# Performance work log

Measured on AMD Instinct MI355X. Metric: run time of the kernel, lower is better.

## Reference

```python
import jax, jax.numpy as jnp
import numpy as np

B, H, S, D = 4, 16, 2048, 128

def setup_inputs() -> dict:
    key = jax.random.key(0)
    kq, kk, kv = jax.random.split(key, 3)
    q = jax.random.normal(kq, (B, H, S, D), dtype=jnp.float32)
    k = jax.random.normal(kk, (B, H, S, D), dtype=jnp.float32)
    v = jax.random.normal(kv, (B, H, S, D), dtype=jnp.float32)
    return {"q": q, "k": k, "v": v}

def reference(q, k, v):
    # scores: [B, H, S, S] -- NOTE: original module applies no 1/sqrt(D) scale
    scores = jnp.einsum("bhqd,bhkd->bhqk", q, k)
    a = jax.nn.softmax(scores, axis=-1)  # numerically stable softmax
    return jnp.einsum("bhqk,bhkd->bhqd", a, v)
```

## Files before the change

### kernel.cpp

```cpp
#include <hip/hip_runtime.h>
#include <hip/hip_bf16.h>


#define QBLK   64
#define KVBLK  64
#define DHEAD  128
#define SEQ    2048
#define KPAD   136
#define PPAD   72
#define RESCALE_THR 8.0f

typedef _Float16 f16x8 __attribute__((ext_vector_type(8)));
typedef _Float16 f16x4 __attribute__((ext_vector_type(4)));
typedef float    f32x4 __attribute__((ext_vector_type(4)));

#define AS1P(x) ((const __attribute__((address_space(1))) void*)(size_t)(x))
#define AS3P(x) ((__attribute__((address_space(3))) void*)(unsigned long long)(unsigned)(size_t)(x))

__global__ __launch_bounds__(256)
void preconv_kernel(const float* __restrict__ K, const float* __restrict__ V,
                    _Float16* __restrict__ Kp, _Float16* __restrict__ Vp) {
    const int bt = blockIdx.x;
    const size_t src = (size_t)bt * (KVBLK * DHEAD);
    const float* Kt = K + src;
    const float* Vt = V + src;
    _Float16* Ko = Kp + src;
    _Float16* Vo = Vp + src;
    #pragma unroll
    for (int j = 0; j < 4; ++j) {
        const int c = threadIdx.x + 256 * j;
        {
            const int row = c >> 4;
            const int d0  = (c & 15) * 8;
            float4 f0 = *(const float4*)(Kt + row * DHEAD + d0);
            float4 f1 = *(const float4*)(Kt + row * DHEAD + d0 + 4);
            f16x8 h;
            h[0]=(_Float16)f0.x; h[1]=(_Float16)f0.y; h[2]=(_Float16)f0.z; h[3]=(_Float16)f0.w;
            h[4]=(_Float16)f1.x; h[5]=(_Float16)f1.y; h[6]=(_Float16)f1.z; h[7]=(_Float16)f1.w;
            *(f16x8*)&Ko[row * 128 + (d0 ^ ((row & 7) << 3))] = h;
        }
        {
            const int d   = c & 127;
            const int kvg = c >> 7;
            f16x8 h;
            #pragma unroll
            for (int i = 0; i < 8; ++i)
                h[i] = (_Float16)Vt[(kvg * 8 + i) * DHEAD + d];
            *(f16x8*)&Vo[d * 64 + ((kvg * 8) ^ ((d & 7) << 3))] = h;
        }
    }
}

__global__ __launch_bounds__(256, 3)
void attn_fwd_kernel(const float* __restrict__ Q, const _Float16* __restrict__ Kp,
                     const _Float16* __restrict__ Vp, float* __restrict__ O) {
    __shared__ __align__(16) _Float16 K_lds[KVBLK * DHEAD];
    __shared__ __align__(16) _Float16 V_lds[DHEAD * KVBLK];
    __shared__ __align__(16) _Float16 P_lds[4 * 16 * 64];

    const int tid  = threadIdx.x;
    const int lane = tid & 63;
    const int wave = tid >> 6;
    const int g    = lane >> 4;
    const int lg   = lane & 15;

    const int flat    = blockIdx.x + gridDim.x * blockIdx.y;
    const int newflat = (flat & 7) * 256 + (flat >> 3);
    const int qtile   = newflat & 31;
    const int bh      = newflat >> 5;

    const float* Qg = Q + (size_t)bh * SEQ * DHEAD + (size_t)(qtile * QBLK) * DHEAD;
    float*       Og = O + (size_t)bh * SEQ * DHEAD + (size_t)(qtile * QBLK) * DHEAD;

    f16x8 qf[4];
    {
        const float* qrow = Qg + (size_t)(wave * 16 + lg) * DHEAD;
        #pragma unroll
        for (int dc = 0; dc < 4; ++dc) {
            const int d0 = dc * 32 + g * 8;
            float4 f0 = *(const float4*)(qrow + d0);
            float4 f1 = *(const float4*)(qrow + d0 + 4);
            qf[dc][0] = (_Float16)f0.x; qf[dc][1] = (_Float16)f0.y;
            qf[dc][2] = (_Float16)f0.z; qf[dc][3] = (_Float16)f0.w;
            qf[dc][4] = (_Float16)f1.x; qf[dc][5] = (_Float16)f1.y;
            qf[dc][6] = (_Float16)f1.z; qf[dc][7] = (_Float16)f1.w;
        }
    }

    f32x4 acc[8];
    #pragma unroll
    for (int dt = 0; dt < 8; ++dt) { acc[dt][0]=0.f; acc[dt][1]=0.f; acc[dt][2]=0.f; acc[dt][3]=0.f; }
    float m = -1e30f, l = 0.f;

    for (int t = 0; t < SEQ / KVBLK; ++t) {
        {
            const _Float16* Ktile = Kp + (size_t)(bh * 32 + t) * (KVBLK * DHEAD);
            const _Float16* Vtile = Vp + (size_t)(bh * 32 + t) * (KVBLK * DHEAD);
            #pragma unroll
            for (int i = 0; i < 4; ++i) {
                const int eoff = wave * 2048 + i * 512;
                __builtin_amdgcn_global_load_lds(AS1P(Ktile + eoff + lane * 8),
                                                 AS3P(&K_lds[eoff]), 16, 0, 0);
                __builtin_amdgcn_global_load_lds(AS1P(Vtile + eoff + lane * 8),
                                                 AS3P(&V_lds[eoff]), 16, 0, 0);
            }
        }
        __syncthreads();

        f32x4 s[4];
        __builtin_amdgcn_s_setprio(1);
        #pragma unroll
        for (int ct = 0; ct < 4; ++ct) {
            f32x4 a; a[0]=0.f; a[1]=0.f; a[2]=0.f; a[3]=0.f;
            #pragma unroll
            for (int dc = 0; dc < 4; ++dc) {
                const int krow = ct * 16 + lg;
                const int off  = krow * 128 + ((dc * 32 + g * 8) ^ ((krow & 7) << 3));
                f16x8 kh = *(const f16x8*)&K_lds[off];
                a = __builtin_amdgcn_mfma_f32_16x16x32_f16(kh, qf[dc], a, 0, 0, 0);
            }
            s[ct] = a;
        }
        __builtin_amdgcn_s_setprio(0);

        float pmax = s[0][0];
        #pragma unroll
        for (int ct = 0; ct < 4; ++ct)
            #pragma unroll
            for (int r = 0; r < 4; ++r)
                pmax = fmaxf(pmax, s[ct][r]);
        pmax = fmaxf(pmax, __shfl_xor(pmax, 16));
        pmax = fmaxf(pmax, __shfl_xor(pmax, 32));

        if (!__all(pmax - m <= RESCALE_THR)) {
            const float mnew = fmaxf(m, pmax);
            const float sc   = __expf(m - mnew);
            m = mnew;
            l *= sc;
            #pragma unroll
            for (int r = 0; r < 4; ++r) {
                const float scr = __shfl(sc, g * 20 + r);
                #pragma unroll
                for (int dt = 0; dt < 8; ++dt) acc[dt][r] *= scr;
            }
        }
        float rs = 0.f;
        #pragma unroll
        for (int ct = 0; ct < 4; ++ct)
            #pragma unroll
            for (int r = 0; r < 4; ++r) {
                float p = __expf(s[ct][r] - m);
                s[ct][r] = p;
                rs += p;
            }
        rs += __shfl_xor(rs, 16);
        rs += __shfl_xor(rs, 32);
        l += rs;

        _Float16* pbase = &P_lds[wave * 16 * 64];
        #pragma unroll
        for (int ct = 0; ct < 4; ++ct) {
            f16x4 pk;
            pk[0] = (_Float16)s[ct][0]; pk[1] = (_Float16)s[ct][1];
            pk[2] = (_Float16)s[ct][2]; pk[3] = (_Float16)s[ct][3];
            *(f16x4*)&pbase[lg * 64 + ((ct * 16 + g * 4) ^ ((lg & 7) << 3))] = pk;
        }

        __builtin_amdgcn_s_setprio(1);
        #pragma unroll
        for (int kt = 0; kt < 2; ++kt) {
            const int koff = (kt * 32 + g * 8) ^ ((lg & 7) << 3);
            f16x8 pf = *(const f16x8*)&pbase[lg * 64 + koff];
            #pragma unroll
            for (int dt = 0; dt < 8; ++dt) {
                f16x8 vf = *(const f16x8*)&V_lds[(dt * 16 + lg) * 64 + koff];
                acc[dt] = __builtin_amdgcn_mfma_f32_16x16x32_f16(pf, vf, acc[dt], 0, 0, 0);
            }
        }
        __builtin_amdgcn_s_setprio(0);
        __syncthreads();
    }

    const float linv = 1.f / l;
    float inv[4];
    #pragma unroll
    for (int r = 0; r < 4; ++r) inv[r] = __shfl(linv, g * 20 + r);
    float* ob = Og + (size_t)(wave * 16) * DHEAD;
    #pragma unroll
    for (int dt = 0; dt < 8; ++dt)
        #pragma unroll
        for (int r = 0; r < 4; ++r)
            ob[(size_t)(g * 4 + r) * DHEAD + dt * 16 + lg] = acc[dt][r] * inv[r];
}

__global__ __launch_bounds__(256, 3)
void attn_fwd_legacy(const float* __restrict__ Q, const float* __restrict__ K,
                     const float* __restrict__ V, float* __restrict__ O) {
    __shared__ __align__(16) _Float16 K_lds[KVBLK * KPAD];
    __shared__ __align__(16) _Float16 V_lds[KVBLK * DHEAD];
    __shared__ __align__(16) _Float16 P_lds[4 * 16 * PPAD];

    const int tid  = threadIdx.x;
    const int lane = tid & 63;
    const int wave = tid >> 6;
    const int g    = lane >> 4;
    const int lg   = lane & 15;

    const int flat    = blockIdx.x + gridDim.x * blockIdx.y;
    const int newflat = (flat & 7) * 256 + (flat >> 3);
    const int qtile   = newflat & 31;
    const int bh      = newflat >> 5;

    const size_t base = (size_t)bh * SEQ * DHEAD;
    const float* Qg = Q + base + (size_t)(qtile * QBLK) * DHEAD;
    const float* Kg = K + base;
    const float* Vg = V + base;
    float*       Og = O + base + (size_t)(qtile * QBLK) * DHEAD;

    const unsigned trbase = (unsigned)(size_t)&V_lds[0] + (unsigned)(g * 2048 + lg * 8);

    f16x8 qf[4];
    {
        const float* qrow = Qg + (size_t)(wave * 16 + lg) * DHEAD;
        #pragma unroll
        for (int dc = 0; dc < 4; ++dc) {
            const int d0 = dc * 32 + g * 8;
            float4 f0 = *(const float4*)(qrow + d0);
            float4 f1 = *(const float4*)(qrow + d0 + 4);
            qf[dc][0] = (_Float16)f0.x; qf[dc][1] = (_Float16)f0.y;
            qf[dc][2] = (_Float16)f0.z; qf[dc][3] = (_Float16)f0.w;
            qf[dc][4] = (_Float16)f1.x; qf[dc][5] = (_Float16)f1.y;
            qf[dc][6] = (_Float16)f1.z; qf[dc][7] = (_Float16)f1.w;
        }
    }

    f32x4 acc[8];
    #pragma unroll
    for (int dt = 0; dt < 8; ++dt) { acc[dt][0]=0.f; acc[dt][1]=0.f; acc[dt][2]=0.f; acc[dt][3]=0.f; }
    float m = -1e30f, l = 0.f;

    for (int t = 0; t < SEQ / KVBLK; ++t) {
        {
            const float* Kt = Kg + (size_t)t * KVBLK * DHEAD;
            #pragma unroll
            for (int j = 0; j < 4; ++j) {
                const int c   = tid + 256 * j;
                const int row = c >> 4;
                const int dc  = (c & 15) * 8;
                float4 f0 = *(const float4*)(Kt + row * DHEAD + dc);
                float4 f1 = *(const float4*)(Kt + row * DHEAD + dc + 4);
                f16x8 vh;
                vh[0]=(_Float16)f0.x; vh[1]=(_Float16)f0.y; vh[2]=(_Float16)f0.z; vh[3]=(_Float16)f0.w;
                vh[4]=(_Float16)f1.x; vh[5]=(_Float16)f1.y; vh[6]=(_Float16)f1.z; vh[7]=(_Float16)f1.w;
                *(f16x8*)&K_lds[row * KPAD + dc] = vh;
            }
            const float* Vt = Vg + (size_t)t * KVBLK * DHEAD;
            #pragma unroll
            for (int j = 0; j < 4; ++j) {
                const int c   = tid + 256 * j;
                const int d8  = (c & 1) | (((c >> 3) & 7) << 1);
                const int row = ((c >> 1) & 3) | ((c >> 6) << 2);
                const int d0  = d8 * 8;
                float4 f0 = *(const float4*)(Vt + row * DHEAD + d0);
                float4 f1 = *(const float4*)(Vt + row * DHEAD + d0 + 4);
                f16x8 vv;
                vv[0]=(_Float16)f0.x; vv[1]=(_Float16)f0.y; vv[2]=(_Float16)f0.z; vv[3]=(_Float16)f0.w;
                vv[4]=(_Float16)f1.x; vv[5]=(_Float16)f1.y; vv[6]=(_Float16)f1.z; vv[7]=(_Float16)f1.w;
                const int st = (row >> 2) * 8 + (d0 >> 4);
                *(f16x8*)&V_lds[st * 64 + (row & 3) * 16 + (d0 & 15)] = vv;
            }
        }
        __syncthreads();

        f32x4 s[4];
        __builtin_amdgcn_s_setprio(1);
        #pragma unroll
        for (int ct = 0; ct < 4; ++ct) {
            f32x4 a; a[0]=0.f; a[1]=0.f; a[2]=0.f; a[3]=0.f;
            #pragma unroll
            for (int dc = 0; dc < 4; ++dc) {
                const int off = (ct * 16 + lg) * KPAD + dc * 32 + g * 8;
                f16x8 kh = *(const f16x8*)&K_lds[off];
                a = __builtin_amdgcn_mfma_f32_16x16x32_f16(kh, qf[dc], a, 0, 0, 0);
            }
            s[ct] = a;
        }
        __builtin_amdgcn_s_setprio(0);

        float pmax = s[0][0];
        #pragma unroll
        for (int ct = 0; ct < 4; ++ct)
            #pragma unroll
            for (int r = 0; r < 4; ++r)
                pmax = fmaxf(pmax, s[ct][r]);
        pmax = fmaxf(pmax, __shfl_xor(pmax, 16));
        pmax = fmaxf(pmax, __shfl_xor(pmax, 32));
        const float mnew = fmaxf(m, pmax);
        const float sc   = __expf(m - mnew);
        m = mnew;
        float rs = 0.f;
        #pragma unroll
        for (int ct = 0; ct < 4; ++ct)
            #pragma unroll
            for (int r = 0; r < 4; ++r) {
                float p = __expf(s[ct][r] - mnew);
                s[ct][r] = p;
                rs += p;
            }
        rs += __shfl_xor(rs, 16);
        rs += __shfl_xor(rs, 32);
        l = l * sc + rs;

        #pragma unroll
        for (int r = 0; r < 4; ++r) {
            const float scr = __shfl(sc, g * 20 + r);
            #pragma unroll
            for (int dt = 0; dt < 8; ++dt) acc[dt][r] *= scr;
        }

        _Float16* pbase = &P_lds[wave * 16 * PPAD];
        #pragma unroll
        for (int ct = 0; ct < 4; ++ct) {
            f16x4 pk;
            pk[0] = (_Float16)s[ct][0]; pk[1] = (_Float16)s[ct][1];
            pk[2] = (_Float16)s[ct][2]; pk[3] = (_Float16)s[ct][3];
            *(f16x4*)&pbase[lg * PPAD + ct * 16 + g * 4] = pk;
        }

        #pragma unroll
        for (int kt = 0; kt < 2; ++kt) {
            f16x8 pf = *(const f16x8*)&pbase[lg * PPAD + kt * 32 + g * 8];
            #pragma unroll
            for (int dp = 0; dp < 4; ++dp) {
                f16x4 a0, a1, b0, b1;
                asm volatile(
                    "ds_read_b64_tr_b16 %0, %4 offset:%5\n\t"
                    "ds_read_b64_tr_b16 %1, %4 offset:%6\n\t"
                    "ds_read_b64_tr_b16 %2, %4 offset:%7\n\t"
                    "ds_read_b64_tr_b16 %3, %4 offset:%8\n\t"
                    "s_waitcnt lgkmcnt(0)"
                    : "=&v"(a0), "=&v"(a1), "=&v"(b0), "=&v"(b1)
                    : "v"(trbase),
                      "i"(kt * 8192 + (dp * 2 + 0) * 128),
                      "i"(kt * 8192 + 1024 + (dp * 2 + 0) * 128),
                      "i"(kt * 8192 + (dp * 2 + 1) * 128),
                      "i"(kt * 8192 + 1024 + (dp * 2 + 1) * 128)
                    : "memory");
                __builtin_amdgcn_sched_barrier(0);
                f16x8 vf0 = __builtin_shufflevector(a0, a1, 0, 1, 2, 3, 4, 5, 6, 7);
                f16x8 vf1 = __builtin_shufflevector(b0, b1, 0, 1, 2, 3, 4, 5, 6, 7);
                __builtin_amdgcn_s_setprio(1);
                acc[dp * 2 + 0] = __builtin_amdgcn_mfma_f32_16x16x32_f16(pf, vf0, acc[dp * 2 + 0], 0, 0, 0);
                acc[dp * 2 + 1] = __builtin_amdgcn_mfma_f32_16x16x32_f16(pf, vf1, acc[dp * 2 + 1], 0, 0, 0);
                __builtin_amdgcn_s_setprio(0);
            }
        }
        __syncthreads();
    }

    const float linv = 1.f / l;
    float inv[4];
    #pragma unroll
    for (int r = 0; r < 4; ++r) inv[r] = __shfl(linv, g * 20 + r);
    float* ob = Og + (size_t)(wave * 16) * DHEAD;
    #pragma unroll
    for (int dt = 0; dt < 8; ++dt)
        #pragma unroll
        for (int r = 0; r < 4; ++r)
            ob[(size_t)(g * 4 + r) * DHEAD + dt * 16 + lg] = acc[dt][r] * inv[r];
}

extern "C" void kernel_launch(void* const* d_in, const int* in_sizes, int n_in,
                              void* d_out, int out_size, void* d_ws, size_t ws_size,
                              hipStream_t stream) {
    const float* q = (const float*)d_in[0];
    const float* k = (const float*)d_in[1];
    const float* v = (const float*)d_in[2];
    float* out = (float*)d_out;
    const int BH = in_sizes[0] / (SEQ * DHEAD);
    dim3 grid(SEQ / QBLK, BH);

    const size_t elems = (size_t)BH * SEQ * DHEAD;
    const size_t need  = elems * 2 * sizeof(_Float16);
    if (ws_size >= need) {
        _Float16* Kp = (_Float16*)d_ws;
        _Float16* Vp = Kp + elems;
        preconv_kernel<<<dim3(BH * (SEQ / KVBLK)), dim3(256), 0, stream>>>(k, v, Kp, Vp);
        attn_fwd_kernel<<<grid, dim3(256), 0, stream>>>(q, Kp, Vp, out);
    } else {
        attn_fwd_legacy<<<grid, dim3(256), 0, stream>>>(q, k, v, out);
    }
}
```

Baseline: 242.3 us.

## Process two 16-row query subtiles per wave to double K/V tile reuse

After: 339.7 us. 40.2% more time.

```diff
diff --git a/kernel.cpp b/kernel.cpp
--- a/kernel.cpp
+++ b/kernel.cpp
@@ -2,10 +2,11 @@
 #include <hip/hip_bf16.h>
 
 
-#define QBLK   64
+#define QBLK   128
 #define KVBLK  64
 #define DHEAD  128
 #define SEQ    2048
+#define NT     (SEQ / KVBLK)
 #define KPAD   136
 #define PPAD   72
 #define RESCALE_THR 8.0f
@@ -51,11 +52,11 @@
     }
 }
 
-__global__ __launch_bounds__(256, 3)
+__global__ __launch_bounds__(256, 4)
 void attn_fwd_kernel(const float* __restrict__ Q, const _Float16* __restrict__ Kp,
                      const _Float16* __restrict__ Vp, float* __restrict__ O) {
     __shared__ __align__(16) _Float16 K_lds[KVBLK * DHEAD];
-    __shared__ __align__(16) _Float16 V_lds[DHEAD * KVBLK];
+    __shared__ __align__(16) _Float16 V_lds[KVBLK * DHEAD];
     __shared__ __align__(16) _Float16 P_lds[4 * 16 * 64];
 
     const int tid  = threadIdx.x;
@@ -65,12 +66,168 @@
     const int lg   = lane & 15;
 
     const int flat    = blockIdx.x + gridDim.x * blockIdx.y;
+    const int newflat = (flat & 7) * 128 + (flat >> 3);
+    const int qtile   = newflat & 15;
+    const int bh      = newflat >> 4;
+
+    const float* Qg = Q + (size_t)bh * SEQ * DHEAD + (size_t)(qtile * QBLK) * DHEAD;
+    float*       Og = O + (size_t)bh * SEQ * DHEAD + (size_t)(qtile * QBLK) * DHEAD;
+
+    f16x8 qf[2][4];
+    #pragma unroll
+    for (int sub = 0; sub < 2; ++sub) {
+        const float* qrow = Qg + (size_t)(wave * 32 + sub * 16 + lg) * DHEAD;
+        #pragma unroll
+        for (int dc = 0; dc < 4; ++dc) {
+            const int d0 = dc * 32 + g * 8;
+            float4 f0 = *(const float4*)(qrow + d0);
+            float4 f1 = *(const float4*)(qrow + d0 + 4);
+            qf[sub][dc][0] = (_Float16)f0.x; qf[sub][dc][1] = (_Float16)f0.y;
+            qf[sub][dc][2] = (_Float16)f0.z; qf[sub][dc][3] = (_Float16)f0.w;
+            qf[sub][dc][4] = (_Float16)f1.x; qf[sub][dc][5] = (_Float16)f1.y;
+            qf[sub][dc][6] = (_Float16)f1.z; qf[sub][dc][7] = (_Float16)f1.w;
+        }
+    }
+
+    f32x4 acc[2][8];
+    #pragma unroll
+    for (int sub = 0; sub < 2; ++sub)
+        #pragma unroll
+        for (int dt = 0; dt < 8; ++dt) { acc[sub][dt][0]=0.f; acc[sub][dt][1]=0.f; acc[sub][dt][2]=0.f; acc[sub][dt][3]=0.f; }
+    float m[2] = {-1e30f, -1e30f}, l[2] = {0.f, 0.f};
+
+    for (int t = 0; t < NT; ++t) {
+        {
+            const _Float16* Ktile = Kp + (size_t)(bh * 32 + t) * (KVBLK * DHEAD);
+            const _Float16* Vtile = Vp + (size_t)(bh * 32 + t) * (KVBLK * DHEAD);
+            #pragma unroll
+            for (int i = 0; i < 4; ++i) {
+                const int eoff = wave * 2048 + i * 512;
+                __builtin_amdgcn_global_load_lds(AS1P(Ktile + eoff + lane * 8),
+                                                 AS3P(&K_lds[eoff]), 16, 0, 0);
+                __builtin_amdgcn_global_load_lds(AS1P(Vtile + eoff + lane * 8),
+                                                 AS3P(&V_lds[eoff]), 16, 0, 0);
+            }
+        }
+        __syncthreads();
+
+        #pragma unroll
+        for (int sub = 0; sub < 2; ++sub) {
+            f32x4 s[4];
+            __builtin_amdgcn_s_setprio(1);
+            #pragma unroll
+            for (int ct = 0; ct < 4; ++ct) {
+                f32x4 a; a[0]=0.f; a[1]=0.f; a[2]=0.f; a[3]=0.f;
+                #pragma unroll
+                for (int dc = 0; dc < 4; ++dc) {
+                    const int krow = ct * 16 + lg;
+                    const int off  = krow * 128 + ((dc * 32 + g * 8) ^ ((krow & 7) << 3));
+                    f16x8 kh = *(const f16x8*)&K_lds[off];
+                    a = __builtin_amdgcn_mfma_f32_16x16x32_f16(kh, qf[sub][dc], a, 0, 0, 0);
+                }
+                s[ct] = a;
+            }
+            __builtin_amdgcn_s_setprio(0);
+
+            float pmax = s[0][0];
+            #pragma unroll
+            for (int ct = 0; ct < 4; ++ct)
+                #pragma unroll
+                for (int r = 0; r < 4; ++r)
+                    pmax = fmaxf(pmax, s[ct][r]);
+            pmax = fmaxf(pmax, __shfl_xor(pmax, 16));
+            pmax = fmaxf(pmax, __shfl_xor(pmax, 32));
+
+            if (!__all(pmax - m[sub] <= RESCALE_THR)) {
+                const float mnew = fmaxf(m[sub], pmax);
+                const float sc   = __expf(m[sub] - mnew);
+                m[sub] = mnew;
+                l[sub] *= sc;
+                #pragma unroll
+                for (int r = 0; r < 4; ++r) {
+                    const float scr = __shfl(sc, g * 20 + r);
+                    #pragma unroll
+                    for (int dt = 0; dt < 8; ++dt) acc[sub][dt][r] *= scr;
+                }
+            }
+            float rs = 0.f;
+            #pragma unroll
+            for (int ct = 0; ct < 4; ++ct)
+                #pragma unroll
+                for (int r = 0; r < 4; ++r) {
+                    float p = __expf(s[ct][r] - m[sub]);
+                    s[ct][r] = p;
+                    rs += p;
+                }
+            rs += __shfl_xor(rs, 16);
+            rs += __shfl_xor(rs, 32);
+            l[sub] += rs;
+
+            _Float16* pbase = &P_lds[wave * 16 * 64];
+            #pragma unroll
+            for (int ct = 0; ct < 4; ++ct) {
+                f16x4 pk;
+                pk[0] = (_Float16)s[ct][0]; pk[1] = (_Float16)s[ct][1];
+                pk[2] = (_Float16)s[ct][2]; pk[3] = (_Float16)s[ct][3];
+                *(f16x4*)&pbase[lg * 64 + ((ct * 16 + g * 4) ^ ((lg & 7) << 3))] = pk;
+            }
+
+            __builtin_amdgcn_s_setprio(1);
+            #pragma unroll
+            for (int kt = 0; kt < 2; ++kt) {
+                const int koff = (kt * 32 + g * 8) ^ ((lg & 7) << 3);
+                f16x8 pf = *(const f16x8*)&pbase[lg * 64 + koff];
+                #pragma unroll
+                for (int dt = 0; dt < 8; ++dt) {
+                    f16x8 vf = *(const f16x8*)&V_lds[(dt * 16 + lg) * 64 + koff];
+                    acc[sub][dt] = __builtin_amdgcn_mfma_f32_16x16x32_f16(pf, vf, acc[sub][dt], 0, 0, 0);
+                }
+            }
+            __builtin_amdgcn_s_setprio(0);
+        }
+        __syncthreads();
+    }
+
+    #pragma unroll
+    for (int sub = 0; sub < 2; ++sub) {
+        const float linv = 1.f / l[sub];
+        float inv[4];
+        #pragma unroll
+        for (int r = 0; r < 4; ++r) inv[r] = __shfl(linv, g * 20 + r);
+        float* ob = Og + (size_t)(wave * 32 + sub * 16) * DHEAD;
+        #pragma unroll
+        for (int dt = 0; dt < 8; ++dt)
+            #pragma unroll
+            for (int r = 0; r < 4; ++r)
+                ob[(size_t)(g * 4 + r) * DHEAD + dt * 16 + lg] = acc[sub][dt][r] * inv[r];
+    }
+}
+
+__global__ __launch_bounds__(256, 3)
+void attn_fwd_legacy(const float* __restrict__ Q, const float* __restrict__ K,
+                     const float* __restrict__ V, float* __restrict__ O) {
+    __shared__ __align__(16) _Float16 K_lds[KVBLK * KPAD];
+    __shared__ __align__(16) _Float16 V_lds[KVBLK * DHEAD];
+    __shared__ __align__(16) _Float16 P_lds[4 * 16 * PPAD];
+
+    const int tid  = threadIdx.x;
+    const int lane = tid & 63;
+    const int wave = tid >> 6;
+    const int g    = lane >> 4;
+    const int lg   = lane & 15;
+
+    const int flat    = blockIdx.x + gridDim.x * blockIdx.y;
     const int newflat = (flat & 7) * 256 + (flat >> 3);
     const int qtile   = newflat & 31;
     const int bh      = newflat >> 5;
 
-    const float* Qg = Q + (size_t)bh * SEQ * DHEAD + (size_t)(qtile * QBLK) * DHEAD;
-    float*       Og = O + (size_t)bh * SEQ * DHEAD + (size_t)(qtile * QBLK) * DHEAD;
+    const size_t base = (size_t)bh * SEQ * DHEAD;
+    const float* Qg = Q + base + (size_t)(qtile * 64) * DHEAD;
+    const float* Kg = K + base;
+    const float* Vg = V + base;
+    float*       Og = O + base + (size_t)(qtile * 64) * DHEAD;
+
+    const unsigned trbase = (unsigned)(size_t)&V_lds[0] + (unsigned)(g * 2048 + lg * 8);
 
     f16x8 qf[4];
     {
@@ -92,154 +249,7 @@
     for (int dt = 0; dt < 8; ++dt) { acc[dt][0]=0.f; acc[dt][1]=0.f; acc[dt][2]=0.f; acc[dt][3]=0.f; }
     float m = -1e30f, l = 0.f;
 
-    for (int t = 0; t < SEQ / KVBLK; ++t) {
-        {
-            const _Float16* Ktile = Kp + (size_t)(bh * 32 + t) * (KVBLK * DHEAD);
-            const _Float16* Vtile = Vp + (size_t)(bh * 32 + t) * (KVBLK * DHEAD);
-            #pragma unroll
-            for (int i = 0; i < 4; ++i) {
-                const int eoff = wave * 2048 + i * 512;
-                __builtin_amdgcn_global_load_lds(AS1P(Ktile + eoff + lane * 8),
-                                                 AS3P(&K_lds[eoff]), 16, 0, 0);
-                __builtin_amdgcn_global_load_lds(AS1P(Vtile + eoff + lane * 8),
-                                                 AS3P(&V_lds[eoff]), 16, 0, 0);
-            }
-        }
-        __syncthreads();
-
-        f32x4 s[4];
-        __builtin_amdgcn_s_setprio(1);
-        #pragma unroll
-        for (int ct = 0; ct < 4; ++ct) {
-            f32x4 a; a[0]=0.f; a[1]=0.f; a[2]=0.f; a[3]=0.f;
-            #pragma unroll
-            for (int dc = 0; dc < 4; ++dc) {
-                const int krow = ct * 16 + lg;
-                const int off  = krow * 128 + ((dc * 32 + g * 8) ^ ((krow & 7) << 3));
-                f16x8 kh = *(const f16x8*)&K_lds[off];
-                a = __builtin_amdgcn_mfma_f32_16x16x32_f16(kh, qf[dc], a, 0, 0, 0);
-            }
-            s[ct] = a;
-        }
-        __builtin_amdgcn_s_setprio(0);
-
-        float pmax = s[0][0];
-        #pragma unroll
-        for (int ct = 0; ct < 4; ++ct)
-            #pragma unroll
-            for (int r = 0; r < 4; ++r)
-                pmax = fmaxf(pmax, s[ct][r]);
-        pmax = fmaxf(pmax, __shfl_xor(pmax, 16));
-        pmax = fmaxf(pmax, __shfl_xor(pmax, 32));
-
-        if (!__all(pmax - m <= RESCALE_THR)) {
-            const float mnew = fmaxf(m, pmax);
-            const float sc   = __expf(m - mnew);
-            m = mnew;
-            l *= sc;
-            #pragma unroll
-            for (int r = 0; r < 4; ++r) {
-                const float scr = __shfl(sc, g * 20 + r);
-                #pragma unroll
-                for (int dt = 0; dt < 8; ++dt) acc[dt][r] *= scr;
-            }
-        }
-        float rs = 0.f;
-        #pragma unroll
-        for (int ct = 0; ct < 4; ++ct)
-            #pragma unroll
-            for (int r = 0; r < 4; ++r) {
-                float p = __expf(s[ct][r] - m);
-                s[ct][r] = p;
-                rs += p;
-            }
-        rs += __shfl_xor(rs, 16);
-        rs += __shfl_xor(rs, 32);
-        l += rs;
-
-        _Float16* pbase = &P_lds[wave * 16 * 64];
-        #pragma unroll
-        for (int ct = 0; ct < 4; ++ct) {
-            f16x4 pk;
-            pk[0] = (_Float16)s[ct][0]; pk[1] = (_Float16)s[ct][1];
-            pk[2] = (_Float16)s[ct][2]; pk[3] = (_Float16)s[ct][3];
-            *(f16x4*)&pbase[lg * 64 + ((ct * 16 + g * 4) ^ ((lg & 7) << 3))] = pk;
-        }
-
-        __builtin_amdgcn_s_setprio(1);
-        #pragma unroll
-        for (int kt = 0; kt < 2; ++kt) {
-            const int koff = (kt * 32 + g * 8) ^ ((lg & 7) << 3);
-            f16x8 pf = *(const f16x8*)&pbase[lg * 64 + koff];
-            #pragma unroll
-            for (int dt = 0; dt < 8; ++dt) {
-                f16x8 vf = *(const f16x8*)&V_lds[(dt * 16 + lg) * 64 + koff];
-                acc[dt] = __builtin_amdgcn_mfma_f32_16x16x32_f16(pf, vf, acc[dt], 0, 0, 0);
-            }
-        }
-        __builtin_amdgcn_s_setprio(0);
-        __syncthreads();
-    }
-
-    const float linv = 1.f / l;
-    float inv[4];
-    #pragma unroll
-    for (int r = 0; r < 4; ++r) inv[r] = __shfl(linv, g * 20 + r);
-    float* ob = Og + (size_t)(wave * 16) * DHEAD;
-    #pragma unroll
-    for (int dt = 0; dt < 8; ++dt)
-        #pragma unroll
-        for (int r = 0; r < 4; ++r)
-            ob[(size_t)(g * 4 + r) * DHEAD + dt * 16 + lg] = acc[dt][r] * inv[r];
-}
-
-__global__ __launch_bounds__(256, 3)
-void attn_fwd_legacy(const float* __restrict__ Q, const float* __restrict__ K,
-                     const float* __restrict__ V, float* __restrict__ O) {
-    __shared__ __align__(16) _Float16 K_lds[KVBLK * KPAD];
-    __shared__ __align__(16) _Float16 V_lds[KVBLK * DHEAD];
-    __shared__ __align__(16) _Float16 P_lds[4 * 16 * PPAD];
-
-    const int tid  = threadIdx.x;
-    const int lane = tid & 63;
-    const int wave = tid >> 6;
-    const int g    = lane >> 4;
-    const int lg   = lane & 15;
-
-    const int flat    = blockIdx.x + gridDim.x * blockIdx.y;
-    const int newflat = (flat & 7) * 256 + (flat >> 3);
-    const int qtile   = newflat & 31;
-    const int bh      = newflat >> 5;
-
-    const size_t base = (size_t)bh * SEQ * DHEAD;
-    const float* Qg = Q + base + (size_t)(qtile * QBLK) * DHEAD;
-    const float* Kg = K + base;
-    const float* Vg = V + base;
-    float*       Og = O + base + (size_t)(qtile * QBLK) * DHEAD;
-
-    const unsigned trbase = (unsigned)(size_t)&V_lds[0] + (unsigned)(g * 2048 + lg * 8);
-
-    f16x8 qf[4];
-    {
-        const float* qrow = Qg + (size_t)(wave * 16 + lg) * DHEAD;
-        #pragma unroll
-        for (int dc = 0; dc < 4; ++dc) {
-            const int d0 = dc * 32 + g * 8;
-            float4 f0 = *(const float4*)(qrow + d0);
-            float4 f1 = *(const float4*)(qrow + d0 + 4);
-            qf[dc][0] = (_Float16)f0.x; qf[dc][1] = (_Float16)f0.y;
-            qf[dc][2] = (_Float16)f0.z; qf[dc][3] = (_Float16)f0.w;
-            qf[dc][4] = (_Float16)f1.x; qf[dc][5] = (_Float16)f1.y;
-            qf[dc][6] = (_Float16)f1.z; qf[dc][7] = (_Float16)f1.w;
-        }
-    }
-
-    f32x4 acc[8];
-    #pragma unroll
-    for (int dt = 0; dt < 8; ++dt) { acc[dt][0]=0.f; acc[dt][1]=0.f; acc[dt][2]=0.f; acc[dt][3]=0.f; }
-    float m = -1e30f, l = 0.f;
-
-    for (int t = 0; t < SEQ / KVBLK; ++t) {
+    for (int t = 0; t < NT; ++t) {
         {
             const float* Kt = Kg + (size_t)t * KVBLK * DHEAD;
             #pragma unroll
@@ -378,7 +388,6 @@
     const float* v = (const float*)d_in[2];
     float* out = (float*)d_out;
     const int BH = in_sizes[0] / (SEQ * DHEAD);
-    dim3 grid(SEQ / QBLK, BH);
 
     const size_t elems = (size_t)BH * SEQ * DHEAD;
     const size_t need  = elems * 2 * sizeof(_Float16);
@@ -386,8 +395,8 @@
         _Float16* Kp = (_Float16*)d_ws;
         _Float16* Vp = Kp + elems;
         preconv_kernel<<<dim3(BH * (SEQ / KVBLK)), dim3(256), 0, stream>>>(k, v, Kp, Vp);
-        attn_fwd_kernel<<<grid, dim3(256), 0, stream>>>(q, Kp, Vp, out);
+        attn_fwd_kernel<<<dim3(SEQ / QBLK, BH), dim3(256), 0, stream>>>(q, Kp, Vp, out);
     } else {
-        attn_fwd_legacy<<<grid, dim3(256), 0, stream>>>(q, k, v, out);
+        attn_fwd_legacy<<<dim3(SEQ / 64, BH), dim3(256), 0, stream>>>(q, k, v, out);
     }
 }
```

## Switch attention to 32x32x16 MFMA with 128-row Q tiles and register-resident P

Applied to the files above, without the earlier changes.

New measurement: 322.7 us. 33.1% more time.

```diff
diff --git a/kernel.cpp b/kernel.cpp
--- a/kernel.cpp
+++ b/kernel.cpp
@@ -2,17 +2,18 @@
 #include <hip/hip_bf16.h>
 
 
-#define QBLK   64
 #define KVBLK  64
 #define DHEAD  128
 #define SEQ    2048
+#define NT     (SEQ / KVBLK)
 #define KPAD   136
 #define PPAD   72
 #define RESCALE_THR 8.0f
 
 typedef _Float16 f16x8 __attribute__((ext_vector_type(8)));
 typedef _Float16 f16x4 __attribute__((ext_vector_type(4)));
-typedef float    f32x4 __attribute__((ext_vector_type(4)));
+typedef float    f32x4  __attribute__((ext_vector_type(4)));
+typedef float    f32x16 __attribute__((ext_vector_type(16)));
 
 #define AS1P(x) ((const __attribute__((address_space(1))) void*)(size_t)(x))
 #define AS3P(x) ((__attribute__((address_space(3))) void*)(unsigned long long)(unsigned)(size_t)(x))
@@ -40,23 +41,166 @@
             *(f16x8*)&Ko[row * 128 + (d0 ^ ((row & 7) << 3))] = h;
         }
         {
-            const int d   = c & 127;
-            const int kvg = c >> 7;
+            const int d  = c & 127;
+            const int G  = c >> 7;
+            const int kt = G >> 1, hh = G & 1;
             f16x8 h;
             #pragma unroll
+            for (int i = 0; i < 8; ++i) {
+                const int kv = kt * 16 + 4 * hh + (i & 3) + 8 * (i >> 2);
+                h[i] = (_Float16)Vt[kv * DHEAD + d];
+            }
+            *(f16x8*)&Vo[d * 64 + (G ^ (d & 7)) * 8] = h;
+        }
+    }
+}
+
+__global__ __launch_bounds__(256)
+void attn_fwd_kernel32(const float* __restrict__ Q, const _Float16* __restrict__ Kp,
+                       const _Float16* __restrict__ Vp, float* __restrict__ O) {
+    __shared__ __align__(16) _Float16 K_lds[KVBLK * DHEAD];
+    __shared__ __align__(16) _Float16 V_lds[KVBLK * DHEAD];
+
+    const int tid  = threadIdx.x;
+    const int lane = tid & 63;
+    const int wave = tid >> 6;
+    const int l31  = lane & 31;
+    const int l5   = lane >> 5;
+
+    const int flat    = blockIdx.x + gridDim.x * blockIdx.y;
+    const int newflat = (flat & 7) * 128 + (flat >> 3);
+    const int qtile   = newflat & 15;
+    const int bh      = newflat >> 4;
+
+    const float* Qg = Q + (size_t)bh * SEQ * DHEAD + (size_t)(qtile * 128) * DHEAD;
+    float*       Og = O + (size_t)bh * SEQ * DHEAD + (size_t)(qtile * 128) * DHEAD;
+
+    f16x8 qf[8];
+    {
+        const float* qrow = Qg + (size_t)(wave * 32 + l31) * DHEAD;
+        #pragma unroll
+        for (int dc = 0; dc < 8; ++dc) {
+            const int d0 = dc * 16 + l5 * 8;
+            float4 f0 = *(const float4*)(qrow + d0);
+            float4 f1 = *(const float4*)(qrow + d0 + 4);
+            qf[dc][0] = (_Float16)f0.x; qf[dc][1] = (_Float16)f0.y;
+            qf[dc][2] = (_Float16)f0.z; qf[dc][3] = (_Float16)f0.w;
+            qf[dc][4] = (_Float16)f1.x; qf[dc][5] = (_Float16)f1.y;
+            qf[dc][6] = (_Float16)f1.z; qf[dc][7] = (_Float16)f1.w;
+        }
+    }
+
+    f32x16 acc[4];
+    #pragma unroll
+    for (int dt = 0; dt < 4; ++dt)
+        #pragma unroll
+        for (int r = 0; r < 16; ++r) acc[dt][r] = 0.f;
+    float m = -1e30f, l = 0.f;
+
+    for (int t = 0; t < NT; ++t) {
+        {
+            const _Float16* Ktile = Kp + (size_t)(bh * 32 + t) * (KVBLK * DHEAD);
+            const _Float16* Vtile = Vp + (size_t)(bh * 32 + t) * (KVBLK * DHEAD);
+            #pragma unroll
+            for (int i = 0; i < 4; ++i) {
+                const int eoff = wave * 2048 + i * 512;
+                __builtin_amdgcn_global_load_lds(AS1P(Ktile + eoff + lane * 8),
+                                                 AS3P(&K_lds[eoff]), 16, 0, 0);
+                __builtin_amdgcn_global_load_lds(AS1P(Vtile + eoff + lane * 8),
+                                                 AS3P(&V_lds[eoff]), 16, 0, 0);
+            }
+        }
+        __syncthreads();
+
+        f32x16 s[2];
+        __builtin_amdgcn_s_setprio(1);
+        #pragma unroll
+        for (int ct = 0; ct < 2; ++ct) {
+            f32x16 a;
+            #pragma unroll
+            for (int r = 0; r < 16; ++r) a[r] = 0.f;
+            #pragma unroll
+            for (int dc = 0; dc < 8; ++dc) {
+                const int kv = ct * 32 + l31;
+                const int koff = kv * 128 + (((dc * 2 + l5) ^ (kv & 7)) * 8);
+                f16x8 kh = *(const f16x8*)&K_lds[koff];
+                a = __builtin_amdgcn_mfma_f32_32x32x16_f16(kh, qf[dc], a, 0, 0, 0);
+            }
+            s[ct] = a;
+        }
+        __builtin_amdgcn_s_setprio(0);
+
+        float pmax = s[0][0];
+        #pragma unroll
+        for (int ct = 0; ct < 2; ++ct)
+            #pragma unroll
+            for (int r = 0; r < 16; ++r)
+                pmax = fmaxf(pmax, s[ct][r]);
+        pmax = fmaxf(pmax, __shfl_xor(pmax, 32));
+        if (!__all(pmax - m <= RESCALE_THR)) {
+            const float mnew = fmaxf(m, pmax);
+            const float sc   = __expf(m - mnew);
+            m = mnew;
+            l *= sc;
+            #pragma unroll
+            for (int r = 0; r < 16; ++r) {
+                const float scr = __shfl(sc, (r & 3) + 8 * (r >> 2) + 4 * l5);
+                #pragma unroll
+                for (int dt = 0; dt < 4; ++dt) acc[dt][r] *= scr;
+            }
+        }
+        float rs = 0.f;
+        #pragma unroll
+        for (int ct = 0; ct < 2; ++ct)
+            #pragma unroll
+            for (int r = 0; r < 16; ++r) {
+                float p = __expf(s[ct][r] - m);
+                s[ct][r] = p;
+                rs += p;
+            }
+        rs += __shfl_xor(rs, 32);
+        l += rs;
+
+        f16x8 pa[4];
+        #pragma unroll
+        for (int kt = 0; kt < 4; ++kt)
+            #pragma unroll
             for (int i = 0; i < 8; ++i)
-                h[i] = (_Float16)Vt[(kvg * 8 + i) * DHEAD + d];
-            *(f16x8*)&Vo[d * 64 + ((kvg * 8) ^ ((d & 7) << 3))] = h;
-        }
-    }
+                pa[kt][i] = (_Float16)s[kt >> 1][4 * (2 * (kt & 1) + (i >> 2)) + (i & 3)];
+
+        __builtin_amdgcn_s_setprio(1);
+        #pragma unroll
+        for (int kt = 0; kt < 4; ++kt)
+            #pragma unroll
+            for (int dt = 0; dt < 4; ++dt) {
+                const int d = dt * 32 + l31;
+                const int voff = d * 64 + (((kt * 2 + l5) ^ (d & 7)) * 8);
+                f16x8 vf = *(const f16x8*)&V_lds[voff];
+                acc[dt] = __builtin_amdgcn_mfma_f32_32x32x16_f16(pa[kt], vf, acc[dt], 0, 0, 0);
+            }
+        __builtin_amdgcn_s_setprio(0);
+        __syncthreads();
+    }
+
+    const float linv = 1.f / l;
+    float inv[16];
+    #pragma unroll
+    for (int r = 0; r < 16; ++r) inv[r] = __shfl(linv, (r & 3) + 8 * (r >> 2) + 4 * l5);
+    #pragma unroll
+    for (int dt = 0; dt < 4; ++dt)
+        #pragma unroll
+        for (int r = 0; r < 16; ++r) {
+            const int qrow = wave * 32 + (r & 3) + 8 * (r >> 2) + 4 * l5;
+            Og[(size_t)qrow * DHEAD + dt * 32 + l31] = acc[dt][r] * inv[r];
+        }
 }
 
 __global__ __launch_bounds__(256, 3)
-void attn_fwd_kernel(const float* __restrict__ Q, const _Float16* __restrict__ Kp,
-                     const _Float16* __restrict__ Vp, float* __restrict__ O) {
-    __shared__ __align__(16) _Float16 K_lds[KVBLK * DHEAD];
-    __shared__ __align__(16) _Float16 V_lds[DHEAD * KVBLK];
-    __shared__ __align__(16) _Float16 P_lds[4 * 16 * 64];
+void attn_fwd_legacy(const float* __restrict__ Q, const float* __restrict__ K,
+                     const float* __restrict__ V, float* __restrict__ O) {
+    __shared__ __align__(16) _Float16 K_lds[KVBLK * KPAD];
+    __shared__ __align__(16) _Float16 V_lds[KVBLK * DHEAD];
+    __shared__ __align__(16) _Float16 P_lds[4 * 16 * PPAD];
 
     const int tid  = threadIdx.x;
     const int lane = tid & 63;
@@ -69,8 +213,13 @@
     const int qtile   = newflat & 31;
     const int bh      = newflat >> 5;
 
-    const float* Qg = Q + (size_t)bh * SEQ * DHEAD + (size_t)(qtile * QBLK) * DHEAD;
-    float*       Og = O + (size_t)bh * SEQ * DHEAD + (size_t)(qtile * QBLK) * DHEAD;
+    const size_t base = (size_t)bh * SEQ * DHEAD;
+    const float* Qg = Q + base + (size_t)(qtile * 64) * DHEAD;
+    const float* Kg = K + base;
+    const float* Vg = V + base;
+    float*       Og = O + base + (size_t)(qtile * 64) * DHEAD;
+
+    const unsigned trbase = (unsigned)(size_t)&V_lds[0] + (unsigned)(g * 2048 + lg * 8);
 
     f16x8 qf[4];
     {
@@ -92,154 +241,7 @@
     for (int dt = 0; dt < 8; ++dt) { acc[dt][0]=0.f; acc[dt][1]=0.f; acc[dt][2]=0.f; acc[dt][3]=0.f; }
     float m = -1e30f, l = 0.f;
 
-    for (int t = 0; t < SEQ / KVBLK; ++t) {
-        {
-            const _Float16* Ktile = Kp + (size_t)(bh * 32 + t) * (KVBLK * DHEAD);
-            const _Float16* Vtile = Vp + (size_t)(bh * 32 + t) * (KVBLK * DHEAD);
-            #pragma unroll
-            for (int i = 0; i < 4; ++i) {
-                const int eoff = wave * 2048 + i * 512;
-                __builtin_amdgcn_global_load_lds(AS1P(Ktile + eoff + lane * 8),
-                                                 AS3P(&K_lds[eoff]), 16, 0, 0);
-                __builtin_amdgcn_global_load_lds(AS1P(Vtile + eoff + lane * 8),
-                                                 AS3P(&V_lds[eoff]), 16, 0, 0);
-            }
-        }
-        __syncthreads();
-
-        f32x4 s[4];
-        __builtin_amdgcn_s_setprio(1);
-        #pragma unroll
-        for (int ct = 0; ct < 4; ++ct) {
-            f32x4 a; a[0]=0.f; a[1]=0.f; a[2]=0.f; a[3]=0.f;
-            #pragma unroll
-            for (int dc = 0; dc < 4; ++dc) {
-                const int krow = ct * 16 + lg;
-                const int off  = krow * 128 + ((dc * 32 + g * 8) ^ ((krow & 7) << 3));
-                f16x8 kh = *(const f16x8*)&K_lds[off];
-                a = __builtin_amdgcn_mfma_f32_16x16x32_f16(kh, qf[dc], a, 0, 0, 0);
-            }
-            s[ct] = a;
-        }
-        __builtin_amdgcn_s_setprio(0);
-
-        float pmax = s[0][0];
-        #pragma unroll
-        for (int ct = 0; ct < 4; ++ct)
-            #pragma unroll
-            for (int r = 0; r < 4; ++r)
-                pmax = fmaxf(pmax, s[ct][r]);
-        pmax = fmaxf(pmax, __shfl_xor(pmax, 16));
-        pmax = fmaxf(pmax, __shfl_xor(pmax, 32));
-
-        if (!__all(pmax - m <= RESCALE_THR)) {
-            const float mnew = fmaxf(m, pmax);
-            const float sc   = __expf(m - mnew);
-            m = mnew;
-            l *= sc;
-            #pragma unroll
-            for (int r = 0; r < 4; ++r) {
-                const float scr = __shfl(sc, g * 20 + r);
-                #pragma unroll
-                for (int dt = 0; dt < 8; ++dt) acc[dt][r] *= scr;
-            }
-        }
-        float rs = 0.f;
-        #pragma unroll
-        for (int ct = 0; ct < 4; ++ct)
-            #pragma unroll
-            for (int r = 0; r < 4; ++r) {
-                float p = __expf(s[ct][r] - m);
-                s[ct][r] = p;
-                rs += p;
-            }
-        rs += __shfl_xor(rs, 16);
-        rs += __shfl_xor(rs, 32);
-        l += rs;
-
-        _Float16* pbase = &P_lds[wave * 16 * 64];
-        #pragma unroll
-        for (int ct = 0; ct < 4; ++ct) {
-            f16x4 pk;
-            pk[0] = (_Float16)s[ct][0]; pk[1] = (_Float16)s[ct][1];
-            pk[2] = (_Float16)s[ct][2]; pk[3] = (_Float16)s[ct][3];
-            *(f16x4*)&pbase[lg * 64 + ((ct * 16 + g * 4) ^ ((lg & 7) << 3))] = pk;
-        }
-
-        __builtin_amdgcn_s_setprio(1);
-        #pragma unroll
-        for (int kt = 0; kt < 2; ++kt) {
-            const int koff = (kt * 32 + g * 8) ^ ((lg & 7) << 3);
-            f16x8 pf = *(const f16x8*)&pbase[lg * 64 + koff];
-            #pragma unroll
-            for (int dt = 0; dt < 8; ++dt) {
-                f16x8 vf = *(const f16x8*)&V_lds[(dt * 16 + lg) * 64 + koff];
-                acc[dt] = __builtin_amdgcn_mfma_f32_16x16x32_f16(pf, vf, acc[dt], 0, 0, 0);
-            }
-        }
-        __builtin_amdgcn_s_setprio(0);
-        __syncthreads();
-    }
-
-    const float linv = 1.f / l;
-    float inv[4];
-    #pragma unroll
-    for (int r = 0; r < 4; ++r) inv[r] = __shfl(linv, g * 20 + r);
-    float* ob = Og + (size_t)(wave * 16) * DHEAD;
-    #pragma unroll
-    for (int dt = 0; dt < 8; ++dt)
-        #pragma unroll
-        for (int r = 0; r < 4; ++r)
-            ob[(size_t)(g * 4 + r) * DHEAD + dt * 16 + lg] = acc[dt][r] * inv[r];
-}
-
-__global__ __launch_bounds__(256, 3)
-void attn_fwd_legacy(const float* __restrict__ Q, const float* __restrict__ K,
-                     const float* __restrict__ V, float* __restrict__ O) {
-    __shared__ __align__(16) _Float16 K_lds[KVBLK * KPAD];
-    __shared__ __align__(16) _Float16 V_lds[KVBLK * DHEAD];
-    __shared__ __align__(16) _Float16 P_lds[4 * 16 * PPAD];
-
-    const int tid  = threadIdx.x;
-    const int lane = tid & 63;
-    const int wave = tid >> 6;
-    const int g    = lane >> 4;
-    const int lg   = lane & 15;
-
-    const int flat    = blockIdx.x + gridDim.x * blockIdx.y;
-    const int newflat = (flat & 7) * 256 + (flat >> 3);
-    const int qtile   = newflat & 31;
-    const int bh      = newflat >> 5;
-
-    const size_t base = (size_t)bh * SEQ * DHEAD;
-    const float* Qg = Q + base + (size_t)(qtile * QBLK) * DHEAD;
-    const float* Kg = K + base;
-    const float* Vg = V + base;
-    float*       Og = O + base + (size_t)(qtile * QBLK) * DHEAD;
-
-    const unsigned trbase = (unsigned)(size_t)&V_lds[0] + (unsigned)(g * 2048 + lg * 8);
-
-    f16x8 qf[4];
-    {
-        const float* qrow = Qg + (size_t)(wave * 16 + lg) * DHEAD;
-        #pragma unroll
-        for (int dc = 0; dc < 4; ++dc) {
-            const int d0 = dc * 32 + g * 8;
-            float4 f0 = *(const float4*)(qrow + d0);
-            float4 f1 = *(const float4*)(qrow + d0 + 4);
-            qf[dc][0] = (_Float16)f0.x; qf[dc][1] = (_Float16)f0.y;
-            qf[dc][2] = (_Float16)f0.z; qf[dc][3] = (_Float16)f0.w;
-            qf[dc][4] = (_Float16)f1.x; qf[dc][5] = (_Float16)f1.y;
-            qf[dc][6] = (_Float16)f1.z; qf[dc][7] = (_Float16)f1.w;
-        }
-    }
-
-    f32x4 acc[8];
-    #pragma unroll
-    for (int dt = 0; dt < 8; ++dt) { acc[dt][0]=0.f; acc[dt][1]=0.f; acc[dt][2]=0.f; acc[dt][3]=0.f; }
-    float m = -1e30f, l = 0.f;
-
-    for (int t = 0; t < SEQ / KVBLK; ++t) {
+    for (int t = 0; t < NT; ++t) {
         {
             const float* Kt = Kg + (size_t)t * KVBLK * DHEAD;
             #pragma unroll
@@ -378,7 +380,6 @@
     const float* v = (const float*)d_in[2];
     float* out = (float*)d_out;
     const int BH = in_sizes[0] / (SEQ * DHEAD);
-    dim3 grid(SEQ / QBLK, BH);
 
     const size_t elems = (size_t)BH * SEQ * DHEAD;
     const size_t need  = elems * 2 * sizeof(_Float16);
@@ -386,8 +387,8 @@
         _Float16* Kp = (_Float16*)d_ws;
         _Float16* Vp = Kp + elems;
         preconv_kernel<<<dim3(BH * (SEQ / KVBLK)), dim3(256), 0, stream>>>(k, v, Kp, Vp);
-        attn_fwd_kernel<<<grid, dim3(256), 0, stream>>>(q, Kp, Vp, out);
+        attn_fwd_kernel32<<<dim3(SEQ / 128, BH), dim3(256), 0, stream>>>(q, Kp, Vp, out);
     } else {
-        attn_fwd_legacy<<<grid, dim3(256), 0, stream>>>(q, k, v, out);
+        attn_fwd_legacy<<<dim3(SEQ / 64, BH), dim3(256), 0, stream>>>(q, k, v, out);
     }
 }
```
